# Kernel optimization log

Measured on AMD Instinct MI355X. Metric: run time of the kernel, lower is better.

## Reference

```python
import jax, jax.numpy as jnp
import numpy as np

N = 50000   # nodes
E = 600000  # edges
D = 128     # in_feats
H = 128     # n_hidden
C = 47      # n_classes


def setup_inputs() -> dict:
    key = jax.random.key(0)
    ks = jax.random.split(key, 12)
    x = jax.random.normal(ks[0], (N, D), dtype=jnp.float32)
    src = jax.random.randint(ks[1], (E,), 0, N, dtype=jnp.int32)
    dst = jax.random.randint(ks[2], (E,), 0, N, dtype=jnp.int32)
    def lin(k, fi, fo):
        s = 1.0 / np.sqrt(fi)
        return jax.random.uniform(k, (fi, fo), jnp.float32, -s, s)
    return {
        "x": x, "src": src, "dst": dst,
        "W_self0": lin(ks[3], D, H), "W_neigh0": lin(ks[4], D, H), "b0": jnp.zeros((H,), jnp.float32),
        "W_self1": lin(ks[5], H, H), "W_neigh1": lin(ks[6], H, H), "b1": jnp.zeros((H,), jnp.float32),
        "W_self2": lin(ks[7], H, C), "W_neigh2": lin(ks[8], H, C), "b2": jnp.zeros((C,), jnp.float32),
    }


def _sage_layer(h, src, dst, W_self, W_neigh, b, act):
    # gather neighbor (src) features, mean-aggregate onto dst nodes
    msum = jax.ops.segment_sum(h[src], dst, num_segments=N)           # [N, F]
    deg = jax.ops.segment_sum(jnp.ones((src.shape[0], 1), h.dtype), dst, num_segments=N)
    h_neigh = msum / jnp.maximum(deg, 1.0)                            # zero-degree -> 0
    out = h @ W_self + h_neigh @ W_neigh + b
    return jax.nn.relu(out) if act else out


def reference(x, src, dst, W_self0, W_neigh0, b0, W_self1, W_neigh1, b1, W_self2, W_neigh2, b2):
    h = _sage_layer(x, src, dst, W_self0, W_neigh0, b0, True)
    h = _sage_layer(h, src, dst, W_self1, W_neigh1, b1, True)
    h = _sage_layer(h, src, dst, W_self2, W_neigh2, b2, False)
    return h
```

## Files before the change

kernel.cpp:

```cpp
#include <hip/hip_runtime.h>
#include <hip/hip_bf16.h>


#define THREADS 256

typedef unsigned short u16;
typedef __attribute__((ext_vector_type(8))) short bf16x8;
typedef __attribute__((ext_vector_type(4))) float f32x4;

__device__ inline u16 f2bf(float f) {
    union { float f; unsigned u; } v; v.f = f;
    unsigned r = (v.u + 0x7FFFu + ((v.u >> 16) & 1u)) >> 16;
    return (u16)r;
}
__device__ inline float bf2f(u16 b) {
    union { unsigned u; float f; } v; v.u = ((unsigned)b) << 16;
    return v.f;
}
__device__ inline unsigned pack2(float a, float b) {
    return (unsigned)f2bf(a) | ((unsigned)f2bf(b) << 16);
}

#define GLDS16(gp, lp)                                                         \
    __builtin_amdgcn_global_load_lds(                                          \
        (const __attribute__((address_space(1))) void*)(gp),                   \
        (__attribute__((address_space(3))) void*)(lp), 16, 0, 0)

__global__ void k_count(const int* __restrict__ dst, int* __restrict__ deg, int E) {
    int e = blockIdx.x * blockDim.x + threadIdx.x;
    if (e < E) atomicAdd(&deg[dst[e]], 1);
}

__global__ void k_scan_block(const int* __restrict__ deg, int* __restrict__ off,
                             int* __restrict__ bsum, int n) {
    __shared__ int s[256];
    int t = threadIdx.x;
    int base = blockIdx.x * 1024 + t * 4;
    int v[4];
#pragma unroll
    for (int i = 0; i < 4; i++) v[i] = (base + i < n) ? deg[base + i] : 0;
    int sum = v[0] + v[1] + v[2] + v[3];
    int val = sum;
    s[t] = val;
    __syncthreads();
    for (int o = 1; o < 256; o <<= 1) {
        int x = (t >= o) ? s[t - o] : 0;
        __syncthreads();
        val += x;
        s[t] = val;
        __syncthreads();
    }
    int run = val - sum;
#pragma unroll
    for (int i = 0; i < 4; i++) {
        if (base + i < n) off[base + i] = run;
        run += v[i];
    }
    if (t == 255) bsum[blockIdx.x] = val;
}

__global__ void k_scan_bsum(int* __restrict__ bsum, int nb) {
    if (threadIdx.x == 0 && blockIdx.x == 0) {
        int acc = 0;
        for (int i = 0; i < nb; i++) { int v = bsum[i]; bsum[i] = acc; acc += v; }
    }
}

__global__ void k_scan_add(int* __restrict__ off, const int* __restrict__ bsum, int n) {
    int t = threadIdx.x;
    int base = blockIdx.x * 1024 + t * 4;
    int add = bsum[blockIdx.x];
#pragma unroll
    for (int i = 0; i < 4; i++)
        if (base + i < n) off[base + i] += add;
}

__global__ void k_fill(const int* __restrict__ src, const int* __restrict__ dst,
                       const int* __restrict__ off, int* __restrict__ cur,
                       int* __restrict__ eidx, int E) {
    int e = blockIdx.x * blockDim.x + threadIdx.x;
    if (e < E) {
        int d = dst[e];
        int p = atomicAdd(&cur[d], 1);
        eidx[off[d] + p] = src[e];
    }
}

__global__ void k_prepX(const float* __restrict__ x, u16* __restrict__ hi,
                        u16* __restrict__ lo, int n32) {
    int i = blockIdx.x * blockDim.x + threadIdx.x;
    if (i >= n32) return;
    float4 v = ((const float4*)x)[i];
    float h0 = bf2f(f2bf(v.x)), h1 = bf2f(f2bf(v.y)), h2 = bf2f(f2bf(v.z)), h3 = bf2f(f2bf(v.w));
    uint2 hp, lp;
    hp.x = pack2(h0, h1); hp.y = pack2(h2, h3);
    lp.x = pack2(v.x - h0, v.y - h1); lp.y = pack2(v.z - h2, v.w - h3);
    ((uint2*)hi)[i] = hp;
    ((uint2*)lo)[i] = lp;
}

__global__ void k_prepW(const float* __restrict__ Ws, const float* __restrict__ Wn,
                        u16* __restrict__ Bthi, u16* __restrict__ Btlo, int fout) {
    int idx = blockIdx.x * blockDim.x + threadIdx.x;
    if (idx >= 128 * 256) return;
    int col = idx >> 8;
    int k = idx & 255;
    float v = 0.f;
    if (col < fout) v = (k < 128) ? Ws[k * fout + col] : Wn[(k - 128) * fout + col];
    u16 h = f2bf(v);
    Bthi[idx] = h;
    Btlo[idx] = f2bf(v - bf2f(h));
}

__global__ void k_aggregate(const u16* __restrict__ hi_in, const int* __restrict__ eidx,
                            const int* __restrict__ off, const int* __restrict__ deg,
                            u16* __restrict__ mhi, u16* __restrict__ mlo, int n) {
    int node = blockIdx.x * 4 + (threadIdx.x >> 6);
    int lane = threadIdx.x & 63;
    if (node >= n) return;
    int cnt = deg[node];
    int base = off[node];
    const unsigned* h1 = (const unsigned*)hi_in;
    float2 acc = make_float2(0.f, 0.f);
    for (int j = 0; j < cnt; j += 8) {
        int s[8];
        float m[8];
#pragma unroll
        for (int u = 0; u < 8; u++) {
            int jj = j + u;
            s[u] = eidx[base + (jj < cnt ? jj : 0)];
            m[u] = (jj < cnt) ? 1.f : 0.f;
        }
        unsigned v[8];
#pragma unroll
        for (int u = 0; u < 8; u++) v[u] = h1[(size_t)s[u] * 64 + lane];
#pragma unroll
        for (int u = 0; u < 8; u++) {
            acc.x = fmaf(m[u], bf2f((u16)(v[u] & 0xffffu)), acc.x);
            acc.y = fmaf(m[u], bf2f((u16)(v[u] >> 16)), acc.y);
        }
    }
    float iv = 1.0f / (float)(cnt > 1 ? cnt : 1);
    float a0 = acc.x * iv, a1 = acc.y * iv;
    float h0 = bf2f(f2bf(a0)), h1v = bf2f(f2bf(a1));
    ((unsigned*)mhi)[(size_t)node * 64 + lane] = pack2(a0, a1);
    ((unsigned*)mlo)[(size_t)node * 64 + lane] = pack2(a0 - h0, a1 - h1v);
}

__global__ __launch_bounds__(256) void k_gemm_mfma(
    const u16* __restrict__ Ahi_s, const u16* __restrict__ Alo_s,
    const u16* __restrict__ Ahi_n, const u16* __restrict__ Alo_n,
    const u16* __restrict__ Bthi, const u16* __restrict__ Btlo,
    const float* __restrict__ bias, float* __restrict__ out_f32,
    u16* __restrict__ out_hi, u16* __restrict__ out_lo, int n, int fout, int relu) {
    __shared__ u16 sAhi[64 * 32];
    __shared__ u16 sAlo[64 * 32];
    __shared__ u16 sBhi[128 * 32];
    __shared__ u16 sBlo[128 * 32];

    int t = threadIdx.x;
    int w = t >> 6;
    int lane = t & 63;
    int wr = w >> 1, wc = w & 1;
    size_t row0 = (size_t)blockIdx.x * 64;

    f32x4 acc[2][4];
#pragma unroll
    for (int r = 0; r < 2; r++)
#pragma unroll
        for (int c = 0; c < 4; c++) acc[r][c] = (f32x4){0.f, 0.f, 0.f, 0.f};

    for (int kk = 0; kk < 256; kk += 32) {
        const u16* Phi = (kk < 128) ? Ahi_s : Ahi_n;
        const u16* Plo = (kk < 128) ? Alo_s : Alo_n;
        int kc = kk & 127;
        __syncthreads();
        {
            int r = w * 16 + (lane >> 2);
            int cb = (lane & 3) * 8;
            GLDS16(Phi + (row0 + r) * 128 + kc + cb, &sAhi[r * 32 + cb]);
            GLDS16(Plo + (row0 + r) * 128 + kc + cb, &sAlo[r * 32 + cb]);
        }
#pragma unroll
        for (int i = 0; i < 2; i++) {
            int c = w * 32 + i * 16 + (lane >> 2);
            int cb = (lane & 3) * 8;
            GLDS16(Bthi + (size_t)c * 256 + kk + cb, &sBhi[c * 32 + cb]);
            GLDS16(Btlo + (size_t)c * 256 + kk + cb, &sBlo[c * 32 + cb]);
        }
        __syncthreads();

        bf16x8 a_hi[2], a_lo[2], b_hi[4], b_lo[4];
        int q8 = (lane >> 4) * 8;
#pragma unroll
        for (int r = 0; r < 2; r++) {
            int ad = (wr * 32 + r * 16 + (lane & 15)) * 32 + q8;
            a_hi[r] = *(const bf16x8*)&sAhi[ad];
            a_lo[r] = *(const bf16x8*)&sAlo[ad];
        }
#pragma unroll
        for (int c = 0; c < 4; c++) {
            int ad = (wc * 64 + c * 16 + (lane & 15)) * 32 + q8;
            b_hi[c] = *(const bf16x8*)&sBhi[ad];
            b_lo[c] = *(const bf16x8*)&sBlo[ad];
        }
#pragma unroll
        for (int r = 0; r < 2; r++)
#pragma unroll
            for (int c = 0; c < 4; c++) {
                acc[r][c] = __builtin_amdgcn_mfma_f32_16x16x32_bf16(
                    a_hi[r], b_hi[c], acc[r][c], 0, 0, 0);
                acc[r][c] = __builtin_amdgcn_mfma_f32_16x16x32_bf16(
                    a_hi[r], b_lo[c], acc[r][c], 0, 0, 0);
                acc[r][c] = __builtin_amdgcn_mfma_f32_16x16x32_bf16(
                    a_lo[r], b_hi[c], acc[r][c], 0, 0, 0);
            }
    }

    int quad = lane >> 4;
    int lcol = lane & 15;
#pragma unroll
    for (int r = 0; r < 2; r++) {
#pragma unroll
        for (int c = 0; c < 4; c++) {
            int col = wc * 64 + c * 16 + lcol;
            float bv = (col < fout) ? bias[col] : 0.f;
#pragma unroll
            for (int g = 0; g < 4; g++) {
                size_t row = row0 + wr * 32 + r * 16 + quad * 4 + g;
                if (row >= (size_t)n || col >= fout) continue;
                float v = acc[r][c][g] + bv;
                if (relu) v = v > 0.f ? v : 0.f;
                if (out_f32) out_f32[row * fout + col] = v;
                if (out_hi) {
                    u16 h = f2bf(v);
                    out_hi[row * 128 + col] = h;
                    out_lo[row * 128 + col] = f2bf(v - bf2f(h));
                }
            }
        }
    }
}

extern "C" void kernel_launch(void* const* d_in, const int* in_sizes, int n_in,
                              void* d_out, int out_size, void* d_ws, size_t ws_size,
                              hipStream_t stream) {
    const float* x = (const float*)d_in[0];
    const int* src = (const int*)d_in[1];
    const int* dst = (const int*)d_in[2];
    const float* Ws0 = (const float*)d_in[3];
    const float* Wn0 = (const float*)d_in[4];
    const float* b0 = (const float*)d_in[5];
    const float* Ws1 = (const float*)d_in[6];
    const float* Wn1 = (const float*)d_in[7];
    const float* b1 = (const float*)d_in[8];
    const float* Ws2 = (const float*)d_in[9];
    const float* Wn2 = (const float*)d_in[10];
    const float* b2 = (const float*)d_in[11];
    float* out = (float*)d_out;

    const int N = in_sizes[0] / 128;
    const int E = in_sizes[1];
    const int Npad = ((N + 63) / 64) * 64;

    char* p = (char*)d_ws;
    u16* P0hi = (u16*)p; p += (size_t)Npad * 128 * 2;
    u16* P0lo = (u16*)p; p += (size_t)Npad * 128 * 2;
    u16* P1hi = (u16*)p; p += (size_t)Npad * 128 * 2;
    u16* P1lo = (u16*)p; p += (size_t)Npad * 128 * 2;
    u16* Mhi = (u16*)p; p += (size_t)Npad * 128 * 2;
    u16* Mlo = (u16*)p; p += (size_t)Npad * 128 * 2;
    u16* Bt0h = (u16*)p; p += 128 * 256 * 2;
    u16* Bt0l = (u16*)p; p += 128 * 256 * 2;
    u16* Bt1h = (u16*)p; p += 128 * 256 * 2;
    u16* Bt1l = (u16*)p; p += 128 * 256 * 2;
    u16* Bt2h = (u16*)p; p += 128 * 256 * 2;
    u16* Bt2l = (u16*)p; p += 128 * 256 * 2;
    int* deg = (int*)p; p += (size_t)N * 4;
    int* off = (int*)p; p += (size_t)N * 4;
    int* cur = (int*)p; p += (size_t)N * 4;
    int* eidx = (int*)p; p += (size_t)E * 4;
    int* bsum = (int*)p;

    const int nbE = (E + THREADS - 1) / THREADS;
    const int nbScan = (N + 1023) / 1024;
    const int nbAgg = (N + 3) / 4;
    const int nbGemm = (N + 63) / 64;
    const int nbPX = (N * 32 + THREADS - 1) / THREADS;
    const int nbPW = (128 * 256 + THREADS - 1) / THREADS;

    hipMemsetAsync(deg, 0, (size_t)N * sizeof(int), stream);
    hipMemsetAsync(cur, 0, (size_t)N * sizeof(int), stream);

    k_count<<<nbE, THREADS, 0, stream>>>(dst, deg, E);
    k_scan_block<<<nbScan, 256, 0, stream>>>(deg, off, bsum, N);
    k_scan_bsum<<<1, 64, 0, stream>>>(bsum, nbScan);
    k_scan_add<<<nbScan, 256, 0, stream>>>(off, bsum, N);
    k_fill<<<nbE, THREADS, 0, stream>>>(src, dst, off, cur, eidx, E);

    k_prepX<<<nbPX, THREADS, 0, stream>>>(x, P0hi, P0lo, N * 32);
    k_prepW<<<nbPW, THREADS, 0, stream>>>(Ws0, Wn0, Bt0h, Bt0l, 128);
    k_prepW<<<nbPW, THREADS, 0, stream>>>(Ws1, Wn1, Bt1h, Bt1l, 128);
    k_prepW<<<nbPW, THREADS, 0, stream>>>(Ws2, Wn2, Bt2h, Bt2l, 47);

    k_aggregate<<<nbAgg, 256, 0, stream>>>(P0hi, eidx, off, deg, Mhi, Mlo, N);
    k_gemm_mfma<<<nbGemm, 256, 0, stream>>>(P0hi, P0lo, Mhi, Mlo, Bt0h, Bt0l, b0,
                                            (float*)nullptr, P1hi, P1lo, N, 128, 1);
    k_aggregate<<<nbAgg, 256, 0, stream>>>(P1hi, eidx, off, deg, Mhi, Mlo, N);
    k_gemm_mfma<<<nbGemm, 256, 0, stream>>>(P1hi, P1lo, Mhi, Mlo, Bt1h, Bt1l, b1,
                                            (float*)nullptr, P0hi, P0lo, N, 128, 1);
    k_aggregate<<<nbAgg, 256, 0, stream>>>(P0hi, eidx, off, deg, Mhi, Mlo, N);
    k_gemm_mfma<<<nbGemm, 256, 0, stream>>>(P0hi, P0lo, Mhi, Mlo, Bt2h, Bt2l, b2,
                                            out, (u16*)nullptr, (u16*)nullptr, N, 47, 0);
}
```

Before: 325.5 us.

## Merge weight-prep launches, wave-parallel bsum scan, two nodes per wave in aggregation

Several changes land together. The three weight-prep kernels become one launch, and the two memsets become one because cur now sits right after deg. The single-thread block-sum scan becomes a 64-lane shuffle scan. The aggregation kernel gives each half-wave its own node with 8-byte loads per lane, which doubles the nodes per block and is meant to raise memory-level parallelism on the gather. The aim is fewer launches, less serial work and better gather throughput, with little risk beyond the changed access pattern.

Measured after the change: 309.2 us. 5.0% less time.

```diff
diff --git a/kernel.cpp b/kernel.cpp
--- a/kernel.cpp
+++ b/kernel.cpp
@@ -60,9 +60,19 @@
 }
 
 __global__ void k_scan_bsum(int* __restrict__ bsum, int nb) {
-    if (threadIdx.x == 0 && blockIdx.x == 0) {
-        int acc = 0;
-        for (int i = 0; i < nb; i++) { int v = bsum[i]; bsum[i] = acc; acc += v; }
+    int lane = threadIdx.x;
+    int carry = 0;
+    for (int start = 0; start < nb; start += 64) {
+        int i = start + lane;
+        int orig = (i < nb) ? bsum[i] : 0;
+        int v = orig;
+#pragma unroll
+        for (int o = 1; o < 64; o <<= 1) {
+            int u = __shfl_up(v, o, 64);
+            if (lane >= o) v += u;
+        }
+        if (i < nb) bsum[i] = carry + v - orig;
+        carry += __shfl(v, 63, 64);
     }
 }
 
@@ -99,29 +109,39 @@
     ((uint2*)lo)[i] = lp;
 }
 
-__global__ void k_prepW(const float* __restrict__ Ws, const float* __restrict__ Wn,
-                        u16* __restrict__ Bthi, u16* __restrict__ Btlo, int fout) {
+__global__ void k_prepW3(const float* __restrict__ Ws0, const float* __restrict__ Wn0,
+                         const float* __restrict__ Ws1, const float* __restrict__ Wn1,
+                         const float* __restrict__ Ws2, const float* __restrict__ Wn2,
+                         u16* __restrict__ Bt) {
     int idx = blockIdx.x * blockDim.x + threadIdx.x;
-    if (idx >= 128 * 256) return;
-    int col = idx >> 8;
-    int k = idx & 255;
+    if (idx >= 3 * 128 * 256) return;
+    int layer = idx >> 15;
+    int within = idx & 32767;
+    int col = within >> 8;
+    int k = within & 255;
+    const float* Ws = (layer == 0) ? Ws0 : (layer == 1) ? Ws1 : Ws2;
+    const float* Wn = (layer == 0) ? Wn0 : (layer == 1) ? Wn1 : Wn2;
+    int fout = (layer == 2) ? 47 : 128;
     float v = 0.f;
     if (col < fout) v = (k < 128) ? Ws[k * fout + col] : Wn[(k - 128) * fout + col];
     u16 h = f2bf(v);
-    Bthi[idx] = h;
-    Btlo[idx] = f2bf(v - bf2f(h));
+    Bt[layer * 65536 + within] = h;
+    Bt[layer * 65536 + 32768 + within] = f2bf(v - bf2f(h));
 }
 
 __global__ void k_aggregate(const u16* __restrict__ hi_in, const int* __restrict__ eidx,
                             const int* __restrict__ off, const int* __restrict__ deg,
                             u16* __restrict__ mhi, u16* __restrict__ mlo, int n) {
-    int node = blockIdx.x * 4 + (threadIdx.x >> 6);
+    int wv = blockIdx.x * 4 + (threadIdx.x >> 6);
     int lane = threadIdx.x & 63;
+    int half = lane >> 5;
+    int hl = lane & 31;
+    int node = wv * 2 + half;
     if (node >= n) return;
     int cnt = deg[node];
     int base = off[node];
-    const unsigned* h1 = (const unsigned*)hi_in;
-    float2 acc = make_float2(0.f, 0.f);
+    const uint2* h2 = (const uint2*)hi_in;
+    float4 acc = make_float4(0.f, 0.f, 0.f, 0.f);
     for (int j = 0; j < cnt; j += 8) {
         int s[8];
         float m[8];
@@ -131,20 +151,25 @@
             s[u] = eidx[base + (jj < cnt ? jj : 0)];
             m[u] = (jj < cnt) ? 1.f : 0.f;
         }
-        unsigned v[8];
-#pragma unroll
-        for (int u = 0; u < 8; u++) v[u] = h1[(size_t)s[u] * 64 + lane];
+        uint2 v[8];
+#pragma unroll
+        for (int u = 0; u < 8; u++) v[u] = h2[(size_t)s[u] * 32 + hl];
 #pragma unroll
         for (int u = 0; u < 8; u++) {
-            acc.x = fmaf(m[u], bf2f((u16)(v[u] & 0xffffu)), acc.x);
-            acc.y = fmaf(m[u], bf2f((u16)(v[u] >> 16)), acc.y);
+            acc.x = fmaf(m[u], bf2f((u16)(v[u].x & 0xffffu)), acc.x);
+            acc.y = fmaf(m[u], bf2f((u16)(v[u].x >> 16)), acc.y);
+            acc.z = fmaf(m[u], bf2f((u16)(v[u].y & 0xffffu)), acc.z);
+            acc.w = fmaf(m[u], bf2f((u16)(v[u].y >> 16)), acc.w);
         }
     }
     float iv = 1.0f / (float)(cnt > 1 ? cnt : 1);
-    float a0 = acc.x * iv, a1 = acc.y * iv;
-    float h0 = bf2f(f2bf(a0)), h1v = bf2f(f2bf(a1));
-    ((unsigned*)mhi)[(size_t)node * 64 + lane] = pack2(a0, a1);
-    ((unsigned*)mlo)[(size_t)node * 64 + lane] = pack2(a0 - h0, a1 - h1v);
+    float a0 = acc.x * iv, a1 = acc.y * iv, a2 = acc.z * iv, a3 = acc.w * iv;
+    float r0 = bf2f(f2bf(a0)), r1 = bf2f(f2bf(a1)), r2 = bf2f(f2bf(a2)), r3 = bf2f(f2bf(a3));
+    uint2 hp, lp;
+    hp.x = pack2(a0, a1); hp.y = pack2(a2, a3);
+    lp.x = pack2(a0 - r0, a1 - r1); lp.y = pack2(a2 - r2, a3 - r3);
+    ((uint2*)mhi)[(size_t)node * 32 + hl] = hp;
+    ((uint2*)mlo)[(size_t)node * 32 + hl] = lp;
 }
 
 __global__ __launch_bounds__(256) void k_gemm_mfma(
@@ -270,27 +295,21 @@
     u16* P1lo = (u16*)p; p += (size_t)Npad * 128 * 2;
     u16* Mhi = (u16*)p; p += (size_t)Npad * 128 * 2;
     u16* Mlo = (u16*)p; p += (size_t)Npad * 128 * 2;
-    u16* Bt0h = (u16*)p; p += 128 * 256 * 2;
-    u16* Bt0l = (u16*)p; p += 128 * 256 * 2;
-    u16* Bt1h = (u16*)p; p += 128 * 256 * 2;
-    u16* Bt1l = (u16*)p; p += 128 * 256 * 2;
-    u16* Bt2h = (u16*)p; p += 128 * 256 * 2;
-    u16* Bt2l = (u16*)p; p += 128 * 256 * 2;
+    u16* Bt = (u16*)p; p += 3 * 2 * 128 * 256 * 2;
     int* deg = (int*)p; p += (size_t)N * 4;
+    int* cur = (int*)p; p += (size_t)N * 4;
     int* off = (int*)p; p += (size_t)N * 4;
-    int* cur = (int*)p; p += (size_t)N * 4;
     int* eidx = (int*)p; p += (size_t)E * 4;
     int* bsum = (int*)p;
 
     const int nbE = (E + THREADS - 1) / THREADS;
     const int nbScan = (N + 1023) / 1024;
-    const int nbAgg = (N + 3) / 4;
+    const int nbAgg = (N + 7) / 8;
     const int nbGemm = (N + 63) / 64;
     const int nbPX = (N * 32 + THREADS - 1) / THREADS;
-    const int nbPW = (128 * 256 + THREADS - 1) / THREADS;
-
-    hipMemsetAsync(deg, 0, (size_t)N * sizeof(int), stream);
-    hipMemsetAsync(cur, 0, (size_t)N * sizeof(int), stream);
+    const int nbPW = (3 * 128 * 256 + THREADS - 1) / THREADS;
+
+    hipMemsetAsync(deg, 0, (size_t)2 * N * sizeof(int), stream);
 
     k_count<<<nbE, THREADS, 0, stream>>>(dst, deg, E);
     k_scan_block<<<nbScan, 256, 0, stream>>>(deg, off, bsum, N);
@@ -299,17 +318,18 @@
     k_fill<<<nbE, THREADS, 0, stream>>>(src, dst, off, cur, eidx, E);
 
     k_prepX<<<nbPX, THREADS, 0, stream>>>(x, P0hi, P0lo, N * 32);
-    k_prepW<<<nbPW, THREADS, 0, stream>>>(Ws0, Wn0, Bt0h, Bt0l, 128);
-    k_prepW<<<nbPW, THREADS, 0, stream>>>(Ws1, Wn1, Bt1h, Bt1l, 128);
-    k_prepW<<<nbPW, THREADS, 0, stream>>>(Ws2, Wn2, Bt2h, Bt2l, 47);
+    k_prepW3<<<nbPW, THREADS, 0, stream>>>(Ws0, Wn0, Ws1, Wn1, Ws2, Wn2, Bt);
 
     k_aggregate<<<nbAgg, 256, 0, stream>>>(P0hi, eidx, off, deg, Mhi, Mlo, N);
-    k_gemm_mfma<<<nbGemm, 256, 0, stream>>>(P0hi, P0lo, Mhi, Mlo, Bt0h, Bt0l, b0,
+    k_gemm_mfma<<<nbGemm, 256, 0, stream>>>(P0hi, P0lo, Mhi, Mlo,
+                                            Bt + 0 * 65536, Bt + 0 * 65536 + 32768, b0,
                                             (float*)nullptr, P1hi, P1lo, N, 128, 1);
     k_aggregate<<<nbAgg, 256, 0, stream>>>(P1hi, eidx, off, deg, Mhi, Mlo, N);
-    k_gemm_mfma<<<nbGemm, 256, 0, stream>>>(P1hi, P1lo, Mhi, Mlo, Bt1h, Bt1l, b1,
+    k_gemm_mfma<<<nbGemm, 256, 0, stream>>>(P1hi, P1lo, Mhi, Mlo,
+                                            Bt + 1 * 65536, Bt + 1 * 65536 + 32768, b1,
                                             (float*)nullptr, P0hi, P0lo, N, 128, 1);
     k_aggregate<<<nbAgg, 256, 0, stream>>>(P0hi, eidx, off, deg, Mhi, Mlo, N);
-    k_gemm_mfma<<<nbGemm, 256, 0, stream>>>(P0hi, P0lo, Mhi, Mlo, Bt2h, Bt2l, b2,
+    k_gemm_mfma<<<nbGemm, 256, 0, stream>>>(P0hi, P0lo, Mhi, Mlo,
+                                            Bt + 2 * 65536, Bt + 2 * 65536 + 32768, b2,
                                             out, (u16*)nullptr, (u16*)nullptr, N, 47, 0);
 }
```
